# Optimization experiments

Hardware: AMD Instinct MI355X
Metric: run time of the kernel (lower is better)

The kernel has to match this reference:

```python
import jax, jax.numpy as jnp
import numpy as np

N = 50000   # nodes
E = 600000  # edges
F = 128     # feat_in
H = 64      # hidden_features
H2 = 32     # hidden_features // 2


def setup_inputs() -> dict:
    key = jax.random.key(0)
    ks = jax.random.split(key, 10)
    w = lambda k, shape: jax.random.normal(k, shape, dtype=jnp.float32) * 0.05
    return {
        "x": jax.random.normal(ks[0], (N, F), dtype=jnp.float32),
        "edge_index": jax.random.randint(ks[1], (2, E), 0, N, dtype=jnp.int32),
        "edge_attr": jax.random.uniform(ks[2], (E, 1), dtype=jnp.float32),
        # GINConv 1 MLP: Linear(F,H) -> Linear(H,H), learnable eps
        "w1a": w(ks[3], (H, F)), "b1a": jnp.zeros((H,), jnp.float32),
        "w1b": w(ks[4], (H, H)), "b1b": jnp.zeros((H,), jnp.float32),
        "eps1": jnp.zeros((), jnp.float32),
        # GINConv 2 MLP: Linear(H,H2) -> Linear(H2,H2), learnable eps
        "w2a": w(ks[5], (H2, H)), "b2a": jnp.zeros((H2,), jnp.float32),
        "w2b": w(ks[6], (H2, H2)), "b2b": jnp.zeros((H2,), jnp.float32),
        "eps2": jnp.zeros((), jnp.float32),
        # SAGEConv(H2, 1): lin_l (neighbor path, has bias), lin_r (root path, no bias)
        "wl": w(ks[7], (1, H2)), "bl": jnp.zeros((1,), jnp.float32),
        "wr": w(ks[8], (1, H2)),
    }


def _gin(x, src, dst, eps, wa, ba, wb, bb):
    # GIN: MLP((1+eps)*x_i + sum_{j->i} x_j)
    agg = jax.ops.segment_sum(x[src], dst, num_segments=x.shape[0])
    h = (1.0 + eps) * x + agg
    h = h @ wa.T + ba
    return h @ wb.T + bb


def reference(x, edge_index, edge_attr, w1a, b1a, w1b, b1b, eps1,
              w2a, b2a, w2b, b2b, eps2, wl, bl, wr):
    src, dst = edge_index[0], edge_index[1]
    ew = edge_attr.squeeze()  # (E,)
    n = x.shape[0]

    h = jax.nn.relu(_gin(x, src, dst, eps1, w1a, b1a, w1b, b1b))
    # dropout is identity in eval mode
    h = jax.nn.relu(_gin(h, src, dst, eps2, w2a, b2a, w2b, b2b))

    # SAGEConv with edge weights: mean over weighted messages + root transform
    msg = ew[:, None] * h[src]                                   # (E, H2)
    num = jax.ops.segment_sum(msg, dst, num_segments=n)          # (N, H2)
    cnt = jax.ops.segment_sum(jnp.ones((msg.shape[0],), h.dtype), dst, num_segments=n)
    mean = num / jnp.maximum(cnt, 1.0)[:, None]
    out = mean @ wl.T + bl + h @ wr.T                            # (N, 1)
    return jax.nn.relu(out)
```

## Files before the change

kernel.cpp:

```cpp
#include <hip/hip_runtime.h>

#define N_NODES 50000
#define N_EDGES 600000
#define F_IN 128
#define H1 64
#define H2 32
#define NBLK ((N_NODES + 255) / 256)
#define PREP_BLOCKS 41
#define CNT_BLOCKS ((N_EDGES / 4 + 255) / 256)

__device__ inline unsigned bf_round(float x) {
  unsigned u = __float_as_uint(x);
  u += 0x7FFFu + ((u >> 16) & 1u);
  return u >> 16;
}
__device__ inline unsigned pack_bf2(float a, float b) {
  return (bf_round(b) << 16) | bf_round(a);
}
__device__ inline float2 unpack_bf2(unsigned u) {
  return make_float2(__uint_as_float(u << 16), __uint_as_float(u & 0xFFFF0000u));
}

__global__ __launch_bounds__(256) void prep_and_count(
    const float* __restrict__ w1a, const float* __restrict__ b1a,
    const float* __restrict__ w1b, const float* __restrict__ b1b,
    const float* __restrict__ w2a, const float* __restrict__ b2a,
    const float* __restrict__ w2b, const float* __restrict__ b2b,
    float* __restrict__ M1, float* __restrict__ c1,
    float* __restrict__ M2, float* __restrict__ c2,
    const int* __restrict__ ei, int* __restrict__ counts) {
  if (blockIdx.x >= PREP_BLOCKS) {
    int t = (blockIdx.x - PREP_BLOCKS) * 256 + threadIdx.x;
    if (t < N_EDGES / 4) {
      int4 d4 = *reinterpret_cast<const int4*>(&ei[N_EDGES + t * 4]);
      atomicAdd(&counts[d4.x], 1);
      atomicAdd(&counts[d4.y], 1);
      atomicAdd(&counts[d4.z], 1);
      atomicAdd(&counts[d4.w], 1);
    }
    return;
  }
  int i = blockIdx.x * 256 + threadIdx.x;
  if (i < F_IN * H1) {
    int f = i >> 6, h = i & 63;
    float s = 0.f;
    for (int m = 0; m < H1; ++m) s += w1a[m * F_IN + f] * w1b[h * H1 + m];
    M1[i] = s;
    return;
  }
  i -= F_IN * H1;
  if (i < H1) {
    float s = b1b[i];
    for (int m = 0; m < H1; ++m) s += b1a[m] * w1b[i * H1 + m];
    c1[i] = s;
    return;
  }
  i -= H1;
  if (i < H1 * H2) {
    int h = i >> 5, o = i & 31;
    float s = 0.f;
    for (int m = 0; m < H2; ++m) s += w2a[m * H1 + h] * w2b[o * H2 + m];
    M2[i] = s;
    return;
  }
  i -= H1 * H2;
  if (i < H2) {
    float s = b2b[i];
    for (int m = 0; m < H2; ++m) s += b2a[m] * w2b[i * H2 + m];
    c2[i] = s;
  }
}

__global__ __launch_bounds__(256) void block_sums(const int* __restrict__ counts,
                                                  int* __restrict__ bsums) {
  __shared__ int s[256];
  int t = threadIdx.x;
  int i = blockIdx.x * 256 + t;
  s[t] = (i < N_NODES) ? counts[i] : 0;
  __syncthreads();
  for (int off = 128; off > 0; off >>= 1) {
    if (t < off) s[t] += s[t + off];
    __syncthreads();
  }
  if (t == 0) bsums[blockIdx.x] = s[0];
}

__global__ __launch_bounds__(256) void scan_bsums(const int* __restrict__ bsums,
                                                  int* __restrict__ boffs,
                                                  int* __restrict__ row_ptr) {
  __shared__ int s[256];
  int t = threadIdx.x;
  int v = (t < NBLK) ? bsums[t] : 0;
  s[t] = v;
  __syncthreads();
  for (int off = 1; off < 256; off <<= 1) {
    int u = (t >= off) ? s[t - off] : 0;
    __syncthreads();
    s[t] += u;
    __syncthreads();
  }
  if (t < NBLK) boffs[t] = s[t] - v;
  if (t == 255) row_ptr[N_NODES] = s[255];
}

__global__ __launch_bounds__(256) void emit_rowptr(const int* __restrict__ counts,
                                                   const int* __restrict__ boffs,
                                                   int* __restrict__ row_ptr,
                                                   int* __restrict__ cursor) {
  __shared__ int s[256];
  int t = threadIdx.x;
  int i = blockIdx.x * 256 + t;
  int v = (i < N_NODES) ? counts[i] : 0;
  s[t] = v;
  __syncthreads();
  for (int off = 1; off < 256; off <<= 1) {
    int u = (t >= off) ? s[t - off] : 0;
    __syncthreads();
    s[t] += u;
    __syncthreads();
  }
  if (i < N_NODES) {
    int ex = boffs[blockIdx.x] + s[t] - v;
    row_ptr[i] = ex;
    cursor[i] = ex;
  }
}

__global__ __launch_bounds__(256) void fill_csr(const int* __restrict__ ei,
                                                const float* __restrict__ ea,
                                                int* __restrict__ cursor,
                                                int2* __restrict__ csr) {
  int e = blockIdx.x * 256 + threadIdx.x;
  if (e >= N_EDGES) return;
  int s = ei[e];
  int d = ei[N_EDGES + e];
  int pos = atomicAdd(&cursor[d], 1);
  csr[pos] = make_int2(s, __float_as_int(ea[e]));
}

__global__ __launch_bounds__(256) void gemm1(const float* __restrict__ x,
                                             const float* __restrict__ M1,
                                             unsigned* __restrict__ ybf) {
  __shared__ float sW[F_IN * H1];
  __shared__ float sX[32][H1];
  int tid = threadIdx.x;
  for (int i = tid; i < F_IN * H1; i += 256) sW[i] = M1[i];

  int row0 = blockIdx.x * 64;
  int tr = tid >> 4;
  int tc = tid & 15;
  int lrow = tid & 63;
  int kgrp = tid >> 6;
  const float* xrow = x + (long long)(row0 + lrow) * F_IN;
  bool rvalid = (row0 + lrow) < N_NODES;

  float acc[4][4] = {{0.f}};

  for (int kc = 0; kc < 4; ++kc) {
    float4 v0 = make_float4(0.f, 0.f, 0.f, 0.f);
    float4 v1 = make_float4(0.f, 0.f, 0.f, 0.f);
    if (rvalid) {
      v0 = *reinterpret_cast<const float4*>(xrow + kc * 32 + kgrp * 8);
      v1 = *reinterpret_cast<const float4*>(xrow + kc * 32 + kgrp * 8 + 4);
    }
    __syncthreads();
    sX[kgrp * 8 + 0][lrow] = v0.x;
    sX[kgrp * 8 + 1][lrow] = v0.y;
    sX[kgrp * 8 + 2][lrow] = v0.z;
    sX[kgrp * 8 + 3][lrow] = v0.w;
    sX[kgrp * 8 + 4][lrow] = v1.x;
    sX[kgrp * 8 + 5][lrow] = v1.y;
    sX[kgrp * 8 + 6][lrow] = v1.z;
    sX[kgrp * 8 + 7][lrow] = v1.w;
    __syncthreads();
#pragma unroll
    for (int k = 0; k < 32; ++k) {
      float4 a = *reinterpret_cast<const float4*>(&sX[k][tr * 4]);
      float4 b = *reinterpret_cast<const float4*>(&sW[(kc * 32 + k) * H1 + tc * 4]);
      acc[0][0] += a.x * b.x; acc[0][1] += a.x * b.y;
      acc[0][2] += a.x * b.z; acc[0][3] += a.x * b.w;
      acc[1][0] += a.y * b.x; acc[1][1] += a.y * b.y;
      acc[1][2] += a.y * b.z; acc[1][3] += a.y * b.w;
      acc[2][0] += a.z * b.x; acc[2][1] += a.z * b.y;
      acc[2][2] += a.z * b.z; acc[2][3] += a.z * b.w;
      acc[3][0] += a.w * b.x; acc[3][1] += a.w * b.y;
      acc[3][2] += a.w * b.z; acc[3][3] += a.w * b.w;
    }
  }
#pragma unroll
  for (int i = 0; i < 4; ++i) {
    int row = row0 + tr * 4 + i;
    if (row < N_NODES) {
      uint2 o;
      o.x = pack_bf2(acc[i][0], acc[i][1]);
      o.y = pack_bf2(acc[i][2], acc[i][3]);
      *reinterpret_cast<uint2*>(&ybf[(long long)row * 32 + tc * 2]) = o;
    }
  }
}

__global__ __launch_bounds__(256) void agg_h(
    const unsigned* __restrict__ ybf, const int* __restrict__ row_ptr,
    const int2* __restrict__ csr, const float* __restrict__ c1,
    const float* __restrict__ eps1p, float* __restrict__ h) {
  int tid = threadIdx.x;
  int node = blockIdx.x * 8 + (tid >> 5);
  if (node >= N_NODES) return;
  int j = tid & 31;
  int start = row_ptr[node], end = row_ptr[node + 1];
  float a0 = 0.f, a1 = 0.f;
  int e = start;
  for (; e + 4 <= end; e += 4) {
    int s0 = csr[e + 0].x;
    int s1 = csr[e + 1].x;
    int s2 = csr[e + 2].x;
    int s3 = csr[e + 3].x;
    float2 u0 = unpack_bf2(ybf[(unsigned)s0 * 32 + j]);
    float2 u1 = unpack_bf2(ybf[(unsigned)s1 * 32 + j]);
    float2 u2 = unpack_bf2(ybf[(unsigned)s2 * 32 + j]);
    float2 u3 = unpack_bf2(ybf[(unsigned)s3 * 32 + j]);
    a0 += (u0.x + u1.x) + (u2.x + u3.x);
    a1 += (u0.y + u1.y) + (u2.y + u3.y);
  }
  float2 t0 = make_float2(0.f, 0.f), t1 = make_float2(0.f, 0.f),
         t2 = make_float2(0.f, 0.f);
  if (e + 0 < end) t0 = unpack_bf2(ybf[(unsigned)csr[e + 0].x * 32 + j]);
  if (e + 1 < end) t1 = unpack_bf2(ybf[(unsigned)csr[e + 1].x * 32 + j]);
  if (e + 2 < end) t2 = unpack_bf2(ybf[(unsigned)csr[e + 2].x * 32 + j]);
  a0 += (t0.x + t1.x) + t2.x;
  a1 += (t0.y + t1.y) + t2.y;
  float eps1 = 1.0f + *eps1p;
  float2 self = unpack_bf2(ybf[(unsigned)node * 32 + j]);
  float2 c = *reinterpret_cast<const float2*>(&c1[2 * j]);
  float2 hv;
  hv.x = fmaxf(eps1 * self.x + a0 + c.x, 0.f);
  hv.y = fmaxf(eps1 * self.y + a1 + c.y, 0.f);
  *reinterpret_cast<float2*>(&h[(long long)node * H1 + 2 * j]) = hv;
}

__global__ __launch_bounds__(256) void gemm2(const float* __restrict__ h,
                                             const float* __restrict__ M2,
                                             unsigned* __restrict__ zbf) {
  __shared__ float sW[H1 * H2];
  __shared__ float sX[H1][64];
  int tid = threadIdx.x;
  for (int i = tid; i < H1 * H2; i += 256) sW[i] = M2[i];

  int row0 = blockIdx.x * 64;
  int lrow = tid & 63;
  int kg = tid >> 6;
  bool rv = (row0 + lrow) < N_NODES;
  float4 v[4] = {};
  if (rv) {
    const float* hr = h + (long long)(row0 + lrow) * H1 + kg * 16;
#pragma unroll
    for (int q = 0; q < 4; ++q) v[q] = *reinterpret_cast<const float4*>(hr + q * 4);
  }
#pragma unroll
  for (int q = 0; q < 4; ++q) {
    sX[kg * 16 + q * 4 + 0][lrow] = v[q].x;
    sX[kg * 16 + q * 4 + 1][lrow] = v[q].y;
    sX[kg * 16 + q * 4 + 2][lrow] = v[q].z;
    sX[kg * 16 + q * 4 + 3][lrow] = v[q].w;
  }
  __syncthreads();
  int tr = tid >> 4;
  int tc = tid & 15;
  float acc[4][2] = {{0.f}};
#pragma unroll
  for (int k = 0; k < H1; ++k) {
    float4 a = *reinterpret_cast<const float4*>(&sX[k][tr * 4]);
    float2 b = *reinterpret_cast<const float2*>(&sW[k * H2 + tc * 2]);
    acc[0][0] += a.x * b.x; acc[0][1] += a.x * b.y;
    acc[1][0] += a.y * b.x; acc[1][1] += a.y * b.y;
    acc[2][0] += a.z * b.x; acc[2][1] += a.z * b.y;
    acc[3][0] += a.w * b.x; acc[3][1] += a.w * b.y;
  }
#pragma unroll
  for (int i = 0; i < 4; ++i) {
    int row = row0 + tr * 4 + i;
    if (row < N_NODES)
      zbf[(long long)row * 16 + tc] = pack_bf2(acc[i][0], acc[i][1]);
  }
}

__global__ __launch_bounds__(256) void gin3(
    const unsigned* __restrict__ zbf, const int* __restrict__ row_ptr,
    const int2* __restrict__ csr, const float* __restrict__ c2,
    const float* __restrict__ eps2p, const float* __restrict__ wl,
    const float* __restrict__ wr, float* __restrict__ p,
    float* __restrict__ r) {
  int tid = blockIdx.x * 256 + threadIdx.x;
  int node = tid >> 4;
  if (node >= N_NODES) return;
  int j = tid & 15;
  int start = row_ptr[node], end = row_ptr[node + 1];
  float a0 = 0.f, a1 = 0.f;
  int e = start;
  for (; e + 4 <= end; e += 4) {
    int s0 = csr[e + 0].x;
    int s1 = csr[e + 1].x;
    int s2 = csr[e + 2].x;
    int s3 = csr[e + 3].x;
    float2 u0 = unpack_bf2(zbf[(unsigned)s0 * 16 + j]);
    float2 u1 = unpack_bf2(zbf[(unsigned)s1 * 16 + j]);
    float2 u2 = unpack_bf2(zbf[(unsigned)s2 * 16 + j]);
    float2 u3 = unpack_bf2(zbf[(unsigned)s3 * 16 + j]);
    a0 += (u0.x + u1.x) + (u2.x + u3.x);
    a1 += (u0.y + u1.y) + (u2.y + u3.y);
  }
  float2 t0 = make_float2(0.f, 0.f), t1 = make_float2(0.f, 0.f),
         t2 = make_float2(0.f, 0.f);
  if (e + 0 < end) t0 = unpack_bf2(zbf[(unsigned)csr[e + 0].x * 16 + j]);
  if (e + 1 < end) t1 = unpack_bf2(zbf[(unsigned)csr[e + 1].x * 16 + j]);
  if (e + 2 < end) t2 = unpack_bf2(zbf[(unsigned)csr[e + 2].x * 16 + j]);
  a0 += (t0.x + t1.x) + t2.x;
  a1 += (t0.y + t1.y) + t2.y;
  float eps2 = 1.0f + *eps2p;
  float2 self = unpack_bf2(zbf[(unsigned)node * 16 + j]);
  float2 c = *reinterpret_cast<const float2*>(&c2[2 * j]);
  float h0 = fmaxf(eps2 * self.x + a0 + c.x, 0.f);
  float h1 = fmaxf(eps2 * self.y + a1 + c.y, 0.f);
  float2 l = *reinterpret_cast<const float2*>(&wl[2 * j]);
  float2 w = *reinterpret_cast<const float2*>(&wr[2 * j]);
  float pd = h0 * l.x + h1 * l.y;
  float rd = h0 * w.x + h1 * w.y;
#pragma unroll
  for (int m = 8; m >= 1; m >>= 1) {
    pd += __shfl_xor(pd, m, 16);
    rd += __shfl_xor(rd, m, 16);
  }
  if (j == 0) {
    p[node] = pd;
    r[node] = rd;
  }
}

__global__ __launch_bounds__(256) void sage_out(
    const int* __restrict__ row_ptr, const int2* __restrict__ csr,
    const float* __restrict__ p, const float* __restrict__ r,
    const float* __restrict__ blp, float* __restrict__ out) {
  int idx = blockIdx.x * 256 + threadIdx.x;
  int node = idx >> 4;
  if (node >= N_NODES) return;
  int l = idx & 15;
  int start = row_ptr[node], end = row_ptr[node + 1];
  float acc = 0.f;
  for (int e = start + l; e < end; e += 16) {
    int2 c = csr[e];
    acc += __int_as_float(c.y) * p[c.x];
  }
#pragma unroll
  for (int m = 8; m >= 1; m >>= 1) acc += __shfl_xor(acc, m, 16);
  if (l == 0) {
    float mean = acc / fmaxf((float)(end - start), 1.0f);
    out[node] = fmaxf(mean + blp[0] + r[node], 0.f);
  }
}

extern "C" void kernel_launch(void* const* d_in, const int* in_sizes, int n_in,
                              void* d_out, int out_size, void* d_ws,
                              size_t ws_size, hipStream_t stream) {
  const float* x = (const float*)d_in[0];
  const int* ei = (const int*)d_in[1];
  const float* ea = (const float*)d_in[2];
  const float* w1a = (const float*)d_in[3];
  const float* b1a = (const float*)d_in[4];
  const float* w1b = (const float*)d_in[5];
  const float* b1b = (const float*)d_in[6];
  const float* eps1 = (const float*)d_in[7];
  const float* w2a = (const float*)d_in[8];
  const float* b2a = (const float*)d_in[9];
  const float* w2b = (const float*)d_in[10];
  const float* b2b = (const float*)d_in[11];
  const float* eps2 = (const float*)d_in[12];
  const float* wl = (const float*)d_in[13];
  const float* bl = (const float*)d_in[14];
  const float* wr = (const float*)d_in[15];
  float* out = (float*)d_out;

  float* ws = (float*)d_ws;
  float* M1 = ws;
  float* c1 = M1 + F_IN * H1;
  float* M2 = c1 + H1;
  float* c2 = M2 + H1 * H2;
  unsigned* ybf = (unsigned*)(c2 + H2);
  float* h = (float*)(ybf + (size_t)N_NODES * 32);
  unsigned* zbf = (unsigned*)(h + (size_t)N_NODES * H1);
  float* p = (float*)(zbf + (size_t)N_NODES * 16);
  float* r = p + N_NODES;
  int2* csr = (int2*)(r + N_NODES);
  int* counts = (int*)(csr + N_EDGES);
  int* cursor = counts + N_NODES;
  int* bsums = cursor + N_NODES;
  int* boffs = bsums + NBLK;
  int* row_ptr = boffs + NBLK;

  hipMemsetAsync(counts, 0, sizeof(int) * (size_t)N_NODES, stream);

  prep_and_count<<<PREP_BLOCKS + CNT_BLOCKS, 256, 0, stream>>>(
      w1a, b1a, w1b, b1b, w2a, b2a, w2b, b2b, M1, c1, M2, c2, ei, counts);

  block_sums<<<NBLK, 256, 0, stream>>>(counts, bsums);
  scan_bsums<<<1, 256, 0, stream>>>(bsums, boffs, row_ptr);
  emit_rowptr<<<NBLK, 256, 0, stream>>>(counts, boffs, row_ptr, cursor);
  fill_csr<<<(N_EDGES + 255) / 256, 256, 0, stream>>>(ei, ea, cursor, csr);

  gemm1<<<(N_NODES + 63) / 64, 256, 0, stream>>>(x, M1, ybf);

  agg_h<<<(N_NODES + 7) / 8, 256, 0, stream>>>(ybf, row_ptr, csr, c1, eps1, h);

  gemm2<<<(N_NODES + 63) / 64, 256, 0, stream>>>(h, M2, zbf);

  gin3<<<(N_NODES * 16 + 255) / 256, 256, 0, stream>>>(zbf, row_ptr, csr, c2,
                                                       eps2, wl, wr, p, r);

  sage_out<<<(N_NODES * 16 + 255) / 256, 256, 0, stream>>>(row_ptr, csr, p, r,
                                                           bl, out);
}
```

Before: 240.1 us.

## Fuse CSR fill into gemm1 launch and fuse layer-1 aggregation with gemm2

Merges the CSR fill into the gemm1 kernel as extra blocks, with four edges handled per thread using vector loads. Fuses the layer-1 neighbor aggregation with the second GEMM: aggregated rows go into swizzled shared memory instead of a global fp32 h buffer. This removes two launches and the full write and read of h. The gather loops are also unrolled to 8 edges for more memory-level parallelism. The cost is lower per-block parallelism in the fused aggregation, since each block serially processes 64 nodes over 8 rounds.

```diff
diff --git a/kernel.cpp b/kernel.cpp
--- a/kernel.cpp
+++ b/kernel.cpp
@@ -8,6 +8,8 @@
 #define NBLK ((N_NODES + 255) / 256)
 #define PREP_BLOCKS 41
 #define CNT_BLOCKS ((N_EDGES / 4 + 255) / 256)
+#define GEMM1_BLOCKS ((N_NODES + 63) / 64)
+#define FILL_BLOCKS ((N_EDGES / 4 + 255) / 256)
 
 __device__ inline unsigned bf_round(float x) {
   unsigned u = __float_as_uint(x);
@@ -126,23 +128,30 @@
   }
 }
 
-__global__ __launch_bounds__(256) void fill_csr(const int* __restrict__ ei,
-                                                const float* __restrict__ ea,
-                                                int* __restrict__ cursor,
-                                                int2* __restrict__ csr) {
-  int e = blockIdx.x * 256 + threadIdx.x;
-  if (e >= N_EDGES) return;
-  int s = ei[e];
-  int d = ei[N_EDGES + e];
-  int pos = atomicAdd(&cursor[d], 1);
-  csr[pos] = make_int2(s, __float_as_int(ea[e]));
-}
-
-__global__ __launch_bounds__(256) void gemm1(const float* __restrict__ x,
-                                             const float* __restrict__ M1,
-                                             unsigned* __restrict__ ybf) {
+__global__ __launch_bounds__(256) void gemm1_fill(
+    const float* __restrict__ x, const float* __restrict__ M1,
+    unsigned* __restrict__ ybf, const int* __restrict__ ei,
+    const float* __restrict__ ea, int* __restrict__ cursor,
+    int2* __restrict__ csr) {
   __shared__ float sW[F_IN * H1];
   __shared__ float sX[32][H1];
+  if (blockIdx.x >= GEMM1_BLOCKS) {
+    int t = (blockIdx.x - GEMM1_BLOCKS) * 256 + threadIdx.x;
+    if (t < N_EDGES / 4) {
+      int4 s4 = *reinterpret_cast<const int4*>(&ei[4 * t]);
+      int4 d4 = *reinterpret_cast<const int4*>(&ei[N_EDGES + 4 * t]);
+      float4 w4 = *reinterpret_cast<const float4*>(&ea[4 * t]);
+      int p0 = atomicAdd(&cursor[d4.x], 1);
+      csr[p0] = make_int2(s4.x, __float_as_int(w4.x));
+      int p1 = atomicAdd(&cursor[d4.y], 1);
+      csr[p1] = make_int2(s4.y, __float_as_int(w4.y));
+      int p2 = atomicAdd(&cursor[d4.z], 1);
+      csr[p2] = make_int2(s4.z, __float_as_int(w4.z));
+      int p3 = atomicAdd(&cursor[d4.w], 1);
+      csr[p3] = make_int2(s4.w, __float_as_int(w4.w));
+    }
+    return;
+  }
   int tid = threadIdx.x;
   for (int i = tid; i < F_IN * H1; i += 256) sW[i] = M1[i];
 
@@ -194,82 +203,83 @@
       uint2 o;
       o.x = pack_bf2(acc[i][0], acc[i][1]);
       o.y = pack_bf2(acc[i][2], acc[i][3]);
-      *reinterpret_cast<uint2*>(&ybf[(long long)row * 32 + tc * 2]) = o;
-    }
-  }
-}
-
-__global__ __launch_bounds__(256) void agg_h(
+      *reinterpret_cast<uint2*>(&ybf[(unsigned)row * 32 + tc * 2]) = o;
+    }
+  }
+}
+
+__global__ __launch_bounds__(256) void gin2f(
     const unsigned* __restrict__ ybf, const int* __restrict__ row_ptr,
-    const int2* __restrict__ csr, const float* __restrict__ c1,
-    const float* __restrict__ eps1p, float* __restrict__ h) {
-  int tid = threadIdx.x;
-  int node = blockIdx.x * 8 + (tid >> 5);
-  if (node >= N_NODES) return;
-  int j = tid & 31;
-  int start = row_ptr[node], end = row_ptr[node + 1];
-  float a0 = 0.f, a1 = 0.f;
-  int e = start;
-  for (; e + 4 <= end; e += 4) {
-    int s0 = csr[e + 0].x;
-    int s1 = csr[e + 1].x;
-    int s2 = csr[e + 2].x;
-    int s3 = csr[e + 3].x;
-    float2 u0 = unpack_bf2(ybf[(unsigned)s0 * 32 + j]);
-    float2 u1 = unpack_bf2(ybf[(unsigned)s1 * 32 + j]);
-    float2 u2 = unpack_bf2(ybf[(unsigned)s2 * 32 + j]);
-    float2 u3 = unpack_bf2(ybf[(unsigned)s3 * 32 + j]);
-    a0 += (u0.x + u1.x) + (u2.x + u3.x);
-    a1 += (u0.y + u1.y) + (u2.y + u3.y);
-  }
-  float2 t0 = make_float2(0.f, 0.f), t1 = make_float2(0.f, 0.f),
-         t2 = make_float2(0.f, 0.f);
-  if (e + 0 < end) t0 = unpack_bf2(ybf[(unsigned)csr[e + 0].x * 32 + j]);
-  if (e + 1 < end) t1 = unpack_bf2(ybf[(unsigned)csr[e + 1].x * 32 + j]);
-  if (e + 2 < end) t2 = unpack_bf2(ybf[(unsigned)csr[e + 2].x * 32 + j]);
-  a0 += (t0.x + t1.x) + t2.x;
-  a1 += (t0.y + t1.y) + t2.y;
-  float eps1 = 1.0f + *eps1p;
-  float2 self = unpack_bf2(ybf[(unsigned)node * 32 + j]);
-  float2 c = *reinterpret_cast<const float2*>(&c1[2 * j]);
-  float2 hv;
-  hv.x = fmaxf(eps1 * self.x + a0 + c.x, 0.f);
-  hv.y = fmaxf(eps1 * self.y + a1 + c.y, 0.f);
-  *reinterpret_cast<float2*>(&h[(long long)node * H1 + 2 * j]) = hv;
-}
-
-__global__ __launch_bounds__(256) void gemm2(const float* __restrict__ h,
-                                             const float* __restrict__ M2,
-                                             unsigned* __restrict__ zbf) {
+    const int2* __restrict__ csr, const float* __restrict__ M2,
+    const float* __restrict__ c1, const float* __restrict__ eps1p,
+    unsigned* __restrict__ zbf) {
   __shared__ float sW[H1 * H2];
-  __shared__ float sX[H1][64];
+  __shared__ float sh[H1][64];
   int tid = threadIdx.x;
   for (int i = tid; i < H1 * H2; i += 256) sW[i] = M2[i];
-
   int row0 = blockIdx.x * 64;
-  int lrow = tid & 63;
-  int kg = tid >> 6;
-  bool rv = (row0 + lrow) < N_NODES;
-  float4 v[4] = {};
-  if (rv) {
-    const float* hr = h + (long long)(row0 + lrow) * H1 + kg * 16;
-#pragma unroll
-    for (int q = 0; q < 4; ++q) v[q] = *reinterpret_cast<const float4*>(hr + q * 4);
-  }
-#pragma unroll
-  for (int q = 0; q < 4; ++q) {
-    sX[kg * 16 + q * 4 + 0][lrow] = v[q].x;
-    sX[kg * 16 + q * 4 + 1][lrow] = v[q].y;
-    sX[kg * 16 + q * 4 + 2][lrow] = v[q].z;
-    sX[kg * 16 + q * 4 + 3][lrow] = v[q].w;
+  float eps1 = 1.0f + *eps1p;
+  int grp = tid >> 5;
+  int j = tid & 31;
+  int swz = (j & 7) << 2;
+  float2 c = *reinterpret_cast<const float2*>(&c1[2 * j]);
+
+  for (int rnd = 0; rnd < 8; ++rnd) {
+    int nl = rnd * 8 + grp;
+    int node = row0 + nl;
+    float a0 = 0.f, a1 = 0.f;
+    if (node < N_NODES) {
+      int start = row_ptr[node], end = row_ptr[node + 1];
+      int e = start;
+      for (; e + 8 <= end; e += 8) {
+        int s0 = csr[e + 0].x; int s1 = csr[e + 1].x;
+        int s2 = csr[e + 2].x; int s3 = csr[e + 3].x;
+        int s4 = csr[e + 4].x; int s5 = csr[e + 5].x;
+        int s6 = csr[e + 6].x; int s7 = csr[e + 7].x;
+        float2 u0 = unpack_bf2(ybf[(unsigned)s0 * 32 + j]);
+        float2 u1 = unpack_bf2(ybf[(unsigned)s1 * 32 + j]);
+        float2 u2 = unpack_bf2(ybf[(unsigned)s2 * 32 + j]);
+        float2 u3 = unpack_bf2(ybf[(unsigned)s3 * 32 + j]);
+        float2 u4 = unpack_bf2(ybf[(unsigned)s4 * 32 + j]);
+        float2 u5 = unpack_bf2(ybf[(unsigned)s5 * 32 + j]);
+        float2 u6 = unpack_bf2(ybf[(unsigned)s6 * 32 + j]);
+        float2 u7 = unpack_bf2(ybf[(unsigned)s7 * 32 + j]);
+        a0 += ((u0.x + u1.x) + (u2.x + u3.x)) + ((u4.x + u5.x) + (u6.x + u7.x));
+        a1 += ((u0.y + u1.y) + (u2.y + u3.y)) + ((u4.y + u5.y) + (u6.y + u7.y));
+      }
+      for (; e + 4 <= end; e += 4) {
+        int s0 = csr[e + 0].x; int s1 = csr[e + 1].x;
+        int s2 = csr[e + 2].x; int s3 = csr[e + 3].x;
+        float2 u0 = unpack_bf2(ybf[(unsigned)s0 * 32 + j]);
+        float2 u1 = unpack_bf2(ybf[(unsigned)s1 * 32 + j]);
+        float2 u2 = unpack_bf2(ybf[(unsigned)s2 * 32 + j]);
+        float2 u3 = unpack_bf2(ybf[(unsigned)s3 * 32 + j]);
+        a0 += (u0.x + u1.x) + (u2.x + u3.x);
+        a1 += (u0.y + u1.y) + (u2.y + u3.y);
+      }
+      float2 t0 = make_float2(0.f, 0.f), t1 = make_float2(0.f, 0.f),
+             t2 = make_float2(0.f, 0.f);
+      if (e + 0 < end) t0 = unpack_bf2(ybf[(unsigned)csr[e + 0].x * 32 + j]);
+      if (e + 1 < end) t1 = unpack_bf2(ybf[(unsigned)csr[e + 1].x * 32 + j]);
+      if (e + 2 < end) t2 = unpack_bf2(ybf[(unsigned)csr[e + 2].x * 32 + j]);
+      a0 += (t0.x + t1.x) + t2.x;
+      a1 += (t0.y + t1.y) + t2.y;
+      float2 self = unpack_bf2(ybf[(unsigned)node * 32 + j]);
+      a0 = fmaxf(eps1 * self.x + a0 + c.x, 0.f);
+      a1 = fmaxf(eps1 * self.y + a1 + c.y, 0.f);
+    }
+    int col = nl ^ swz;
+    sh[2 * j][col] = a0;
+    sh[2 * j + 1][col] = a1;
   }
   __syncthreads();
-  int tr = tid >> 4;
-  int tc = tid & 15;
+
+  int tr = tid >> 4, tc = tid & 15;
   float acc[4][2] = {{0.f}};
 #pragma unroll
   for (int k = 0; k < H1; ++k) {
-    float4 a = *reinterpret_cast<const float4*>(&sX[k][tr * 4]);
+    int sk = ((k >> 1) & 7) << 2;
+    float4 a = *reinterpret_cast<const float4*>(&sh[k][(tr * 4) ^ sk]);
     float2 b = *reinterpret_cast<const float2*>(&sW[k * H2 + tc * 2]);
     acc[0][0] += a.x * b.x; acc[0][1] += a.x * b.y;
     acc[1][0] += a.y * b.x; acc[1][1] += a.y * b.y;
@@ -280,7 +290,7 @@
   for (int i = 0; i < 4; ++i) {
     int row = row0 + tr * 4 + i;
     if (row < N_NODES)
-      zbf[(long long)row * 16 + tc] = pack_bf2(acc[i][0], acc[i][1]);
+      zbf[(unsigned)row * 16 + tc] = pack_bf2(acc[i][0], acc[i][1]);
   }
 }
 
@@ -297,11 +307,25 @@
   int start = row_ptr[node], end = row_ptr[node + 1];
   float a0 = 0.f, a1 = 0.f;
   int e = start;
+  for (; e + 8 <= end; e += 8) {
+    int s0 = csr[e + 0].x; int s1 = csr[e + 1].x;
+    int s2 = csr[e + 2].x; int s3 = csr[e + 3].x;
+    int s4 = csr[e + 4].x; int s5 = csr[e + 5].x;
+    int s6 = csr[e + 6].x; int s7 = csr[e + 7].x;
+    float2 u0 = unpack_bf2(zbf[(unsigned)s0 * 16 + j]);
+    float2 u1 = unpack_bf2(zbf[(unsigned)s1 * 16 + j]);
+    float2 u2 = unpack_bf2(zbf[(unsigned)s2 * 16 + j]);
+    float2 u3 = unpack_bf2(zbf[(unsigned)s3 * 16 + j]);
+    float2 u4 = unpack_bf2(zbf[(unsigned)s4 * 16 + j]);
+    float2 u5 = unpack_bf2(zbf[(unsigned)s5 * 16 + j]);
+    float2 u6 = unpack_bf2(zbf[(unsigned)s6 * 16 + j]);
+    float2 u7 = unpack_bf2(zbf[(unsigned)s7 * 16 + j]);
+    a0 += ((u0.x + u1.x) + (u2.x + u3.x)) + ((u4.x + u5.x) + (u6.x + u7.x));
+    a1 += ((u0.y + u1.y) + (u2.y + u3.y)) + ((u4.y + u5.y) + (u6.y + u7.y));
+  }
   for (; e + 4 <= end; e += 4) {
-    int s0 = csr[e + 0].x;
-    int s1 = csr[e + 1].x;
-    int s2 = csr[e + 2].x;
-    int s3 = csr[e + 3].x;
+    int s0 = csr[e + 0].x; int s1 = csr[e + 1].x;
+    int s2 = csr[e + 2].x; int s3 = csr[e + 3].x;
     float2 u0 = unpack_bf2(zbf[(unsigned)s0 * 16 + j]);
     float2 u1 = unpack_bf2(zbf[(unsigned)s1 * 16 + j]);
     float2 u2 = unpack_bf2(zbf[(unsigned)s2 * 16 + j]);
@@ -385,8 +409,7 @@
   float* M2 = c1 + H1;
   float* c2 = M2 + H1 * H2;
   unsigned* ybf = (unsigned*)(c2 + H2);
-  float* h = (float*)(ybf + (size_t)N_NODES * 32);
-  unsigned* zbf = (unsigned*)(h + (size_t)N_NODES * H1);
+  unsigned* zbf = ybf + (size_t)N_NODES * 32;
   float* p = (float*)(zbf + (size_t)N_NODES * 16);
   float* r = p + N_NODES;
   int2* csr = (int2*)(r + N_NODES);
@@ -404,13 +427,12 @@
   block_sums<<<NBLK, 256, 0, stream>>>(counts, bsums);
   scan_bsums<<<1, 256, 0, stream>>>(bsums, boffs, row_ptr);
   emit_rowptr<<<NBLK, 256, 0, stream>>>(counts, boffs, row_ptr, cursor);
-  fill_csr<<<(N_EDGES + 255) / 256, 256, 0, stream>>>(ei, ea, cursor, csr);
-
-  gemm1<<<(N_NODES + 63) / 64, 256, 0, stream>>>(x, M1, ybf);
-
-  agg_h<<<(N_NODES + 7) / 8, 256, 0, stream>>>(ybf, row_ptr, csr, c1, eps1, h);
-
-  gemm2<<<(N_NODES + 63) / 64, 256, 0, stream>>>(h, M2, zbf);
+
+  gemm1_fill<<<GEMM1_BLOCKS + FILL_BLOCKS, 256, 0, stream>>>(
+      x, M1, ybf, ei, ea, cursor, csr);
+
+  gin2f<<<(N_NODES + 63) / 64, 256, 0, stream>>>(ybf, row_ptr, csr, M2, c1,
+                                                 eps1, zbf);
 
   gin3<<<(N_NODES * 16 + 255) / 256, 256, 0, stream>>>(zbf, row_ptr, csr, c2,
                                                        eps2, wl, wr, p, r);
```

New measurement: 282.1 us. 1.17x slower.

## Fuse CSR fill into gemm1 launch, split agg_h edges across half-waves, unroll gin3

Applied to the files above, without the earlier changes.

Merges the CSR fill kernel into the gemm1 launch as extra blocks. This removes one launch and lets the atomic scatter run alongside the dense GEMM, and each fill thread now handles four edges with vectorised loads. agg_h now gives each node a full 64-lane wave, with the two halves splitting the edge list and combining through a shuffle, to get more memory-level parallelism per node. gin3 gets an 8-way unrolled gather loop, and some 64-bit index math becomes 32-bit. The costs are idle half-waves in agg_h's epilogue and shared memory reserved by fill blocks that never use it.

```diff
diff --git a/kernel.cpp b/kernel.cpp
--- a/kernel.cpp
+++ b/kernel.cpp
@@ -8,6 +8,8 @@
 #define NBLK ((N_NODES + 255) / 256)
 #define PREP_BLOCKS 41
 #define CNT_BLOCKS ((N_EDGES / 4 + 255) / 256)
+#define GEMM1_BLOCKS ((N_NODES + 63) / 64)
+#define FILL_BLOCKS ((N_EDGES / 4 + 255) / 256)
 
 __device__ inline unsigned bf_round(float x) {
   unsigned u = __float_as_uint(x);
@@ -126,23 +128,30 @@
   }
 }
 
-__global__ __launch_bounds__(256) void fill_csr(const int* __restrict__ ei,
-                                                const float* __restrict__ ea,
-                                                int* __restrict__ cursor,
-                                                int2* __restrict__ csr) {
-  int e = blockIdx.x * 256 + threadIdx.x;
-  if (e >= N_EDGES) return;
-  int s = ei[e];
-  int d = ei[N_EDGES + e];
-  int pos = atomicAdd(&cursor[d], 1);
-  csr[pos] = make_int2(s, __float_as_int(ea[e]));
-}
-
-__global__ __launch_bounds__(256) void gemm1(const float* __restrict__ x,
-                                             const float* __restrict__ M1,
-                                             unsigned* __restrict__ ybf) {
+__global__ __launch_bounds__(256) void gemm1_fill(
+    const float* __restrict__ x, const float* __restrict__ M1,
+    unsigned* __restrict__ ybf, const int* __restrict__ ei,
+    const float* __restrict__ ea, int* __restrict__ cursor,
+    int2* __restrict__ csr) {
   __shared__ float sW[F_IN * H1];
   __shared__ float sX[32][H1];
+  if (blockIdx.x >= GEMM1_BLOCKS) {
+    int t = (blockIdx.x - GEMM1_BLOCKS) * 256 + threadIdx.x;
+    if (t < N_EDGES / 4) {
+      int4 s4 = *reinterpret_cast<const int4*>(&ei[4 * t]);
+      int4 d4 = *reinterpret_cast<const int4*>(&ei[N_EDGES + 4 * t]);
+      float4 w4 = *reinterpret_cast<const float4*>(&ea[4 * t]);
+      int p0 = atomicAdd(&cursor[d4.x], 1);
+      csr[p0] = make_int2(s4.x, __float_as_int(w4.x));
+      int p1 = atomicAdd(&cursor[d4.y], 1);
+      csr[p1] = make_int2(s4.y, __float_as_int(w4.y));
+      int p2 = atomicAdd(&cursor[d4.z], 1);
+      csr[p2] = make_int2(s4.z, __float_as_int(w4.z));
+      int p3 = atomicAdd(&cursor[d4.w], 1);
+      csr[p3] = make_int2(s4.w, __float_as_int(w4.w));
+    }
+    return;
+  }
   int tid = threadIdx.x;
   for (int i = tid; i < F_IN * H1; i += 256) sW[i] = M1[i];
 
@@ -194,7 +203,7 @@
       uint2 o;
       o.x = pack_bf2(acc[i][0], acc[i][1]);
       o.y = pack_bf2(acc[i][2], acc[i][3]);
-      *reinterpret_cast<uint2*>(&ybf[(long long)row * 32 + tc * 2]) = o;
+      *reinterpret_cast<uint2*>(&ybf[(unsigned)row * 32 + tc * 2]) = o;
     }
   }
 }
@@ -204,13 +213,18 @@
     const int2* __restrict__ csr, const float* __restrict__ c1,
     const float* __restrict__ eps1p, float* __restrict__ h) {
   int tid = threadIdx.x;
-  int node = blockIdx.x * 8 + (tid >> 5);
+  int node = blockIdx.x * 4 + (tid >> 6);
   if (node >= N_NODES) return;
-  int j = tid & 31;
+  int lane = tid & 63;
+  int half = lane >> 5;
+  int j = lane & 31;
   int start = row_ptr[node], end = row_ptr[node + 1];
+  int mid = start + ((end - start + 1) >> 1);
+  int b0 = half ? mid : start;
+  int b1 = half ? end : mid;
   float a0 = 0.f, a1 = 0.f;
-  int e = start;
-  for (; e + 4 <= end; e += 4) {
+  int e = b0;
+  for (; e + 4 <= b1; e += 4) {
     int s0 = csr[e + 0].x;
     int s1 = csr[e + 1].x;
     int s2 = csr[e + 2].x;
@@ -224,18 +238,22 @@
   }
   float2 t0 = make_float2(0.f, 0.f), t1 = make_float2(0.f, 0.f),
          t2 = make_float2(0.f, 0.f);
-  if (e + 0 < end) t0 = unpack_bf2(ybf[(unsigned)csr[e + 0].x * 32 + j]);
-  if (e + 1 < end) t1 = unpack_bf2(ybf[(unsigned)csr[e + 1].x * 32 + j]);
-  if (e + 2 < end) t2 = unpack_bf2(ybf[(unsigned)csr[e + 2].x * 32 + j]);
+  if (e + 0 < b1) t0 = unpack_bf2(ybf[(unsigned)csr[e + 0].x * 32 + j]);
+  if (e + 1 < b1) t1 = unpack_bf2(ybf[(unsigned)csr[e + 1].x * 32 + j]);
+  if (e + 2 < b1) t2 = unpack_bf2(ybf[(unsigned)csr[e + 2].x * 32 + j]);
   a0 += (t0.x + t1.x) + t2.x;
   a1 += (t0.y + t1.y) + t2.y;
-  float eps1 = 1.0f + *eps1p;
-  float2 self = unpack_bf2(ybf[(unsigned)node * 32 + j]);
-  float2 c = *reinterpret_cast<const float2*>(&c1[2 * j]);
-  float2 hv;
-  hv.x = fmaxf(eps1 * self.x + a0 + c.x, 0.f);
-  hv.y = fmaxf(eps1 * self.y + a1 + c.y, 0.f);
-  *reinterpret_cast<float2*>(&h[(long long)node * H1 + 2 * j]) = hv;
+  a0 += __shfl_xor(a0, 32);
+  a1 += __shfl_xor(a1, 32);
+  if (half == 0) {
+    float eps1 = 1.0f + *eps1p;
+    float2 self = unpack_bf2(ybf[(unsigned)node * 32 + j]);
+    float2 c = *reinterpret_cast<const float2*>(&c1[2 * j]);
+    float2 hv;
+    hv.x = fmaxf(eps1 * self.x + a0 + c.x, 0.f);
+    hv.y = fmaxf(eps1 * self.y + a1 + c.y, 0.f);
+    *reinterpret_cast<float2*>(&h[(unsigned)node * H1 + 2 * j]) = hv;
+  }
 }
 
 __global__ __launch_bounds__(256) void gemm2(const float* __restrict__ h,
@@ -280,7 +298,7 @@
   for (int i = 0; i < 4; ++i) {
     int row = row0 + tr * 4 + i;
     if (row < N_NODES)
-      zbf[(long long)row * 16 + tc] = pack_bf2(acc[i][0], acc[i][1]);
+      zbf[(unsigned)row * 16 + tc] = pack_bf2(acc[i][0], acc[i][1]);
   }
 }
 
@@ -297,11 +315,25 @@
   int start = row_ptr[node], end = row_ptr[node + 1];
   float a0 = 0.f, a1 = 0.f;
   int e = start;
+  for (; e + 8 <= end; e += 8) {
+    int s0 = csr[e + 0].x; int s1 = csr[e + 1].x;
+    int s2 = csr[e + 2].x; int s3 = csr[e + 3].x;
+    int s4 = csr[e + 4].x; int s5 = csr[e + 5].x;
+    int s6 = csr[e + 6].x; int s7 = csr[e + 7].x;
+    float2 u0 = unpack_bf2(zbf[(unsigned)s0 * 16 + j]);
+    float2 u1 = unpack_bf2(zbf[(unsigned)s1 * 16 + j]);
+    float2 u2 = unpack_bf2(zbf[(unsigned)s2 * 16 + j]);
+    float2 u3 = unpack_bf2(zbf[(unsigned)s3 * 16 + j]);
+    float2 u4 = unpack_bf2(zbf[(unsigned)s4 * 16 + j]);
+    float2 u5 = unpack_bf2(zbf[(unsigned)s5 * 16 + j]);
+    float2 u6 = unpack_bf2(zbf[(unsigned)s6 * 16 + j]);
+    float2 u7 = unpack_bf2(zbf[(unsigned)s7 * 16 + j]);
+    a0 += ((u0.x + u1.x) + (u2.x + u3.x)) + ((u4.x + u5.x) + (u6.x + u7.x));
+    a1 += ((u0.y + u1.y) + (u2.y + u3.y)) + ((u4.y + u5.y) + (u6.y + u7.y));
+  }
   for (; e + 4 <= end; e += 4) {
-    int s0 = csr[e + 0].x;
-    int s1 = csr[e + 1].x;
-    int s2 = csr[e + 2].x;
-    int s3 = csr[e + 3].x;
+    int s0 = csr[e + 0].x; int s1 = csr[e + 1].x;
+    int s2 = csr[e + 2].x; int s3 = csr[e + 3].x;
     float2 u0 = unpack_bf2(zbf[(unsigned)s0 * 16 + j]);
     float2 u1 = unpack_bf2(zbf[(unsigned)s1 * 16 + j]);
     float2 u2 = unpack_bf2(zbf[(unsigned)s2 * 16 + j]);
@@ -404,11 +436,11 @@
   block_sums<<<NBLK, 256, 0, stream>>>(counts, bsums);
   scan_bsums<<<1, 256, 0, stream>>>(bsums, boffs, row_ptr);
   emit_rowptr<<<NBLK, 256, 0, stream>>>(counts, boffs, row_ptr, cursor);
-  fill_csr<<<(N_EDGES + 255) / 256, 256, 0, stream>>>(ei, ea, cursor, csr);
-
-  gemm1<<<(N_NODES + 63) / 64, 256, 0, stream>>>(x, M1, ybf);
-
-  agg_h<<<(N_NODES + 7) / 8, 256, 0, stream>>>(ybf, row_ptr, csr, c1, eps1, h);
+
+  gemm1_fill<<<GEMM1_BLOCKS + FILL_BLOCKS, 256, 0, stream>>>(
+      x, M1, ybf, ei, ea, cursor, csr);
+
+  agg_h<<<(N_NODES + 3) / 4, 256, 0, stream>>>(ybf, row_ptr, csr, c1, eps1, h);
 
   gemm2<<<(N_NODES + 63) / 64, 256, 0, stream>>>(h, M2, zbf);
 
```

Measured after the change: 223.9 us. 6.7% less time.
